# Performance work log

Measured on AMD Instinct MI355X. Metric: run time of the kernel, lower is better.

Reference implementation:

```python
import jax, jax.numpy as jnp
import numpy as np

N_NODES = 50000
N_EDGES = 800000
D_IN, D_HID, D_OUT = 128, 128, 64
BN_EPS = 1e-5


def gcn_conv(x, W, b, src, dst, ew, n):
    # PyG GCNConv: out[i] = sum_j norm_ij * (x @ W)[j] + b, with self-loops added
    xw = x @ W                                   # [N, D_out]
    loop = jnp.arange(n)
    s = jnp.concatenate([src, loop])             # add self-loops (weight 1)
    d = jnp.concatenate([dst, loop])
    w = jnp.concatenate([ew, jnp.ones((n,), x.dtype)])
    deg = jax.ops.segment_sum(w, d, num_segments=n)
    dinv = jnp.where(deg > 0, jax.lax.rsqrt(deg), 0.0)
    norm = dinv[s] * w * dinv[d]                 # symmetric normalization
    msg = xw[s] * norm[:, None]                  # gather + scale  [E+N, D_out]
    return jax.ops.segment_sum(msg, d, num_segments=n) + b


def setup_inputs() -> dict:
    key = jax.random.key(0)
    ks = jax.random.split(key, 12)
    x = jax.random.normal(ks[0], (N_NODES, D_IN), dtype=jnp.float32)
    edge_index = jax.random.randint(ks[1], (2, N_EDGES), 0, N_NODES, dtype=jnp.int64)
    edge_weight = jax.random.uniform(ks[2], (N_EDGES,), dtype=jnp.float32)
    W1 = jax.random.normal(ks[3], (D_IN, D_HID), dtype=jnp.float32) * 0.05
    b1 = jnp.zeros((D_HID,), jnp.float32)
    gamma = jnp.ones((D_HID,), jnp.float32)
    beta = jnp.zeros((D_HID,), jnp.float32)
    running_mean = jax.random.normal(ks[4], (D_HID,), dtype=jnp.float32) * 0.1
    running_var = jax.random.uniform(ks[5], (D_HID,), dtype=jnp.float32) + 0.5
    W2 = jax.random.normal(ks[6], (D_HID, D_OUT), dtype=jnp.float32) * 0.05
    b2 = jnp.zeros((D_OUT,), jnp.float32)
    return {"x": x, "edge_index": edge_index, "edge_weight": edge_weight,
            "W1": W1, "b1": b1, "gamma": gamma, "beta": beta,
            "running_mean": running_mean, "running_var": running_var,
            "W2": W2, "b2": b2}


def reference(x, edge_index, edge_weight, W1, b1, gamma, beta,
              running_mean, running_var, W2, b2):
    src, dst = edge_index[0], edge_index[1]
    n = x.shape[0]
    h = gcn_conv(x, W1, b1, src, dst, edge_weight, n)
    # BatchNorm1d in eval mode (running stats); dropout inactive in eval
    h = (h - running_mean) * jax.lax.rsqrt(running_var + BN_EPS) * gamma + beta
    h = jax.nn.relu(h)
    out = gcn_conv(h, W2, b2, src, dst, edge_weight, n)
    return out
```

## Files before the change

### kernel.cpp

```cpp
#include <hip/hip_runtime.h>
#include <hip/hip_fp16.h>

#define BN_EPS 1e-5f
#define PAD 64

static __device__ __forceinline__ unsigned short f2bf(float f) {
    unsigned u = __float_as_uint(f);
    u += 0x7FFF + ((u >> 16) & 1);
    return (unsigned short)(u >> 16);
}
static __device__ __forceinline__ float bf2f(unsigned short b) {
    return __uint_as_float((unsigned)b << 16);
}
static __device__ __forceinline__ unsigned pk(int s, float w) {
    return ((unsigned)s << 16) | (unsigned)__half_as_ushort(__float2half_rn(w));
}
static __device__ __forceinline__ float pw(unsigned e) {
    return __half2float(__ushort_as_half((unsigned short)(e & 0xFFFFu)));
}

__global__ __launch_bounds__(256) void k_fused(const int* __restrict__ src, const int* __restrict__ dst,
                                               const float* __restrict__ ew,
                                               int* cnt, unsigned* __restrict__ pad, int e, int gfill, int stride,
                                               const float* __restrict__ A, const float* __restrict__ W,
                                               unsigned short* __restrict__ C, int n,
                                               const float* __restrict__ b1, const float* __restrict__ gamma,
                                               const float* __restrict__ beta, const float* __restrict__ mean,
                                               const float* __restrict__ var,
                                               float* __restrict__ bnscale, float* __restrict__ bnshift,
                                               const float* __restrict__ W2, unsigned short* __restrict__ w2bf) {
    __shared__ float WsQ[32 * 128];
    __shared__ float AsT[128 * 32];
    int tid = threadIdx.x;
    int b = (int)blockIdx.x;
    int gGemm = (n + 31) / 32;

    bool isFill = ((b % stride) == 0) && (b / stride < gfill);
    if (isFill) {
        int i0 = ((b / stride) * 256 + tid) * 8;
        if (i0 + 7 < e) {
            int4   s0 = *(const int4*)(src + i0), s1 = *(const int4*)(src + i0 + 4);
            int4   d0 = *(const int4*)(dst + i0), d1 = *(const int4*)(dst + i0 + 4);
            float4 w0 = *(const float4*)(ew + i0), w1 = *(const float4*)(ew + i0 + 4);
            int p0 = atomicAdd(&cnt[d0.x], 1);
            int p1 = atomicAdd(&cnt[d0.y], 1);
            int p2 = atomicAdd(&cnt[d0.z], 1);
            int p3 = atomicAdd(&cnt[d0.w], 1);
            int p4 = atomicAdd(&cnt[d1.x], 1);
            int p5 = atomicAdd(&cnt[d1.y], 1);
            int p6 = atomicAdd(&cnt[d1.z], 1);
            int p7 = atomicAdd(&cnt[d1.w], 1);
            if (p0 < PAD) pad[(size_t)d0.x * PAD + p0] = pk(s0.x, w0.x);
            if (p1 < PAD) pad[(size_t)d0.y * PAD + p1] = pk(s0.y, w0.y);
            if (p2 < PAD) pad[(size_t)d0.z * PAD + p2] = pk(s0.z, w0.z);
            if (p3 < PAD) pad[(size_t)d0.w * PAD + p3] = pk(s0.w, w0.w);
            if (p4 < PAD) pad[(size_t)d1.x * PAD + p4] = pk(s1.x, w1.x);
            if (p5 < PAD) pad[(size_t)d1.y * PAD + p5] = pk(s1.y, w1.y);
            if (p6 < PAD) pad[(size_t)d1.z * PAD + p6] = pk(s1.z, w1.z);
            if (p7 < PAD) pad[(size_t)d1.w * PAD + p7] = pk(s1.w, w1.w);
        } else {
            for (int i = i0; i < e; ++i) {
                int d = dst[i];
                int p = atomicAdd(&cnt[d], 1);
                if (p < PAD) pad[(size_t)d * PAD + p] = pk(src[i], ew[i]);
            }
        }
        return;
    }

    int fillsBefore = (b == 0) ? 0 : min(gfill, (b - 1) / stride + 1);
    int g = b - fillsBefore;
    if (g == gGemm) {
        if (tid < 128) {
            float sc = gamma[tid] * rsqrtf(var[tid] + BN_EPS);
            bnscale[tid] = sc;
            bnshift[tid] = (b1[tid] - mean[tid]) * sc + beta[tid];
        }
        const float4* W4 = (const float4*)W2;
        ushort4* O = (ushort4*)w2bf;
        #pragma unroll
        for (int q = 0; q < 8; ++q) {
            float4 v = W4[q * 256 + tid];
            O[q * 256 + tid] = make_ushort4(f2bf(v.x), f2bf(v.y), f2bf(v.z), f2bf(v.w));
        }
        return;
    }

    int row0 = g * 32;
    {
        int lr = tid & 31, kq = tid >> 5;
        int gr = row0 + lr; if (gr > n - 1) gr = n - 1;
        const float4* A4 = (const float4*)(A + (size_t)gr * 128);
        #pragma unroll
        for (int j = 0; j < 4; ++j) {
            float4 v = A4[kq * 4 + j];
            int k = kq * 16 + j * 4;
            AsT[(k + 0) * 32 + lr] = v.x;
            AsT[(k + 1) * 32 + lr] = v.y;
            AsT[(k + 2) * 32 + lr] = v.z;
            AsT[(k + 3) * 32 + lr] = v.w;
        }
    }
    int cg_ = tid & 31, rg = tid >> 5;
    float4 acc0 = make_float4(0, 0, 0, 0), acc1 = acc0, acc2 = acc0, acc3 = acc0;
    const float4* W4 = (const float4*)W;
    float4* WsQ4 = (float4*)WsQ;
    const float4* AsT4 = (const float4*)AsT;
    for (int ph = 0; ph < 4; ++ph) {
        __syncthreads();
        #pragma unroll
        for (int j = 0; j < 4; ++j)
            WsQ4[j * 256 + tid] = W4[ph * 1024 + j * 256 + tid];
        __syncthreads();
        #pragma unroll 16
        for (int kk = 0; kk < 32; ++kk) {
            float4 w = WsQ4[kk * 32 + cg_];
            float4 a = AsT4[(ph * 32 + kk) * 8 + rg];
            acc0.x += a.x * w.x; acc0.y += a.x * w.y; acc0.z += a.x * w.z; acc0.w += a.x * w.w;
            acc1.x += a.y * w.x; acc1.y += a.y * w.y; acc1.z += a.y * w.z; acc1.w += a.y * w.w;
            acc2.x += a.z * w.x; acc2.y += a.z * w.y; acc2.z += a.z * w.z; acc2.w += a.z * w.w;
            acc3.x += a.w * w.x; acc3.y += a.w * w.y; acc3.z += a.w * w.z; acc3.w += a.w * w.w;
        }
    }
    ushort4* C4 = (ushort4*)C;
    int r = row0 + rg * 4;
    if (r + 0 < n) C4[(size_t)(r + 0) * 32 + cg_] = make_ushort4(f2bf(acc0.x), f2bf(acc0.y), f2bf(acc0.z), f2bf(acc0.w));
    if (r + 1 < n) C4[(size_t)(r + 1) * 32 + cg_] = make_ushort4(f2bf(acc1.x), f2bf(acc1.y), f2bf(acc1.z), f2bf(acc1.w));
    if (r + 2 < n) C4[(size_t)(r + 2) * 32 + cg_] = make_ushort4(f2bf(acc2.x), f2bf(acc2.y), f2bf(acc2.z), f2bf(acc2.w));
    if (r + 3 < n) C4[(size_t)(r + 3) * 32 + cg_] = make_ushort4(f2bf(acc3.x), f2bf(acc3.y), f2bf(acc3.z), f2bf(acc3.w));
}

__global__ __launch_bounds__(256) void k_deg(const int* __restrict__ cnt, const unsigned* __restrict__ pad,
                                             float* __restrict__ dinv, int n) {
    int i = blockIdx.x * 256 + threadIdx.x;
    if (i < n) {
        int c = min(cnt[i], PAD);
        size_t base = (size_t)i * PAD;
        const uint4* row = (const uint4*)(pad + base);
        float s = 1.0f;
        int p = 0;
        for (; p + 3 < c; p += 4) {
            uint4 v = row[p >> 2];
            s += pw(v.x) + pw(v.y) + pw(v.z) + pw(v.w);
        }
        for (; p < c; ++p) s += pw(pad[base + p]);
        dinv[i] = rsqrtf(s);
    }
}

__global__ __launch_bounds__(256) void k_ag12(const unsigned short* __restrict__ xw, const int* __restrict__ cnt,
                                              const unsigned* __restrict__ pad,
                                              const float* __restrict__ dinv,
                                              const float* __restrict__ scale, const float* __restrict__ shift,
                                              const unsigned short* __restrict__ w2bf,
                                              unsigned short* __restrict__ hw2, int n) {
    __shared__ unsigned short W2s[128 * 64];
    int tid = threadIdx.x;
    {
        const uint4* s4 = (const uint4*)w2bf;
        uint4* d4 = (uint4*)W2s;
        #pragma unroll
        for (int q = 0; q < 4; ++q) d4[q * 256 + tid] = s4[q * 256 + tid];
    }
    __syncthreads();

    int g = tid >> 5;
    int lc = tid & 31;
    int node = blockIdx.x * 8 + g;
    if (node >= n) return;

    unsigned hu0, hu1;
    {
        const ushort4* X4 = (const ushort4*)xw;
        float di = dinv[node];
        int c = min(cnt[node], PAD);
        size_t base = (size_t)node * PAD;
        ushort4 q0 = X4[(size_t)node * 32 + lc];
        float4 acc0 = make_float4(bf2f(q0.x) * di, bf2f(q0.y) * di, bf2f(q0.z) * di, bf2f(q0.w) * di);
        float4 acc1 = make_float4(0, 0, 0, 0);
        float4 acc2 = make_float4(0, 0, 0, 0);
        float4 acc3 = make_float4(0, 0, 0, 0);
        int p = 0;
        for (; p + 3 < c; p += 4) {
            uint4 ee = *(const uint4*)(pad + base + p);
            float w0 = pw(ee.x) * dinv[ee.x >> 16];
            float w1 = pw(ee.y) * dinv[ee.y >> 16];
            float w2 = pw(ee.z) * dinv[ee.z >> 16];
            float w3 = pw(ee.w) * dinv[ee.w >> 16];
            ushort4 a = X4[(size_t)(ee.x >> 16) * 32 + lc];
            ushort4 b = X4[(size_t)(ee.y >> 16) * 32 + lc];
            ushort4 gg = X4[(size_t)(ee.z >> 16) * 32 + lc];
            ushort4 d = X4[(size_t)(ee.w >> 16) * 32 + lc];
            acc0.x += w0 * bf2f(a.x); acc0.y += w0 * bf2f(a.y); acc0.z += w0 * bf2f(a.z); acc0.w += w0 * bf2f(a.w);
            acc1.x += w1 * bf2f(b.x); acc1.y += w1 * bf2f(b.y); acc1.z += w1 * bf2f(b.z); acc1.w += w1 * bf2f(b.w);
            acc2.x += w2 * bf2f(gg.x); acc2.y += w2 * bf2f(gg.y); acc2.z += w2 * bf2f(gg.z); acc2.w += w2 * bf2f(gg.w);
            acc3.x += w3 * bf2f(d.x); acc3.y += w3 * bf2f(d.y); acc3.z += w3 * bf2f(d.z); acc3.w += w3 * bf2f(d.w);
        }
        for (; p < c; ++p) {
            unsigned e0 = pad[base + p];
            float w0 = pw(e0) * dinv[e0 >> 16];
            ushort4 a = X4[(size_t)(e0 >> 16) * 32 + lc];
            acc0.x += w0 * bf2f(a.x); acc0.y += w0 * bf2f(a.y); acc0.z += w0 * bf2f(a.z); acc0.w += w0 * bf2f(a.w);
        }
        acc0.x = (acc0.x + acc1.x + acc2.x + acc3.x) * di;
        acc0.y = (acc0.y + acc1.y + acc2.y + acc3.y) * di;
        acc0.z = (acc0.z + acc1.z + acc2.z + acc3.z) * di;
        acc0.w = (acc0.w + acc1.w + acc2.w + acc3.w) * di;
        float4 Sc = ((const float4*)scale)[lc];
        float4 Sh = ((const float4*)shift)[lc];
        unsigned short r0 = f2bf(fmaxf(acc0.x * Sc.x + Sh.x, 0.0f));
        unsigned short r1 = f2bf(fmaxf(acc0.y * Sc.y + Sh.y, 0.0f));
        unsigned short r2 = f2bf(fmaxf(acc0.z * Sc.z + Sh.z, 0.0f));
        unsigned short r3 = f2bf(fmaxf(acc0.w * Sc.w + Sh.w, 0.0f));
        hu0 = ((unsigned)r1 << 16) | (unsigned)r0;
        hu1 = ((unsigned)r3 << 16) | (unsigned)r2;
    }

    float a0 = 0.0f, a1 = 0.0f;
    const unsigned* W2u = (const unsigned*)W2s;
    #pragma unroll 8
    for (int k = 0; k < 32; ++k) {
        unsigned p0 = (unsigned)__shfl((int)hu0, k, 32);
        unsigned p1 = (unsigned)__shfl((int)hu1, k, 32);
        float h0 = bf2f((unsigned short)(p0 & 0xFFFFu));
        float h1 = bf2f((unsigned short)(p0 >> 16));
        float h2 = bf2f((unsigned short)(p1 & 0xFFFFu));
        float h3 = bf2f((unsigned short)(p1 >> 16));
        unsigned w0u = W2u[(4 * k + 0) * 32 + lc];
        unsigned w1u = W2u[(4 * k + 1) * 32 + lc];
        unsigned w2u = W2u[(4 * k + 2) * 32 + lc];
        unsigned w3u = W2u[(4 * k + 3) * 32 + lc];
        a0 += h0 * bf2f((unsigned short)(w0u & 0xFFFFu));
        a1 += h0 * bf2f((unsigned short)(w0u >> 16));
        a0 += h1 * bf2f((unsigned short)(w1u & 0xFFFFu));
        a1 += h1 * bf2f((unsigned short)(w1u >> 16));
        a0 += h2 * bf2f((unsigned short)(w2u & 0xFFFFu));
        a1 += h2 * bf2f((unsigned short)(w2u >> 16));
        a0 += h3 * bf2f((unsigned short)(w3u & 0xFFFFu));
        a1 += h3 * bf2f((unsigned short)(w3u >> 16));
    }
    unsigned outp = ((unsigned)f2bf(a1) << 16) | (unsigned)f2bf(a0);
    ((unsigned*)hw2)[(size_t)node * 32 + lc] = outp;
}

__global__ __launch_bounds__(256) void k_agg2(const unsigned short* __restrict__ hw, const int* __restrict__ cnt,
                                              const unsigned* __restrict__ pad,
                                              const float* __restrict__ dinv,
                                              const float* __restrict__ b2, float* __restrict__ out, int n) {
    int node = blockIdx.x * 16 + (threadIdx.x >> 4);
    if (node >= n) return;
    int lc = threadIdx.x & 15;
    const ushort4* X4 = (const ushort4*)hw;
    float di = dinv[node];
    int c = min(cnt[node], PAD);
    size_t base = (size_t)node * PAD;
    ushort4 q0 = X4[(size_t)node * 16 + lc];
    float4 acc0 = make_float4(bf2f(q0.x) * di, bf2f(q0.y) * di, bf2f(q0.z) * di, bf2f(q0.w) * di);
    float4 acc1 = make_float4(0, 0, 0, 0);
    float4 acc2 = make_float4(0, 0, 0, 0);
    float4 acc3 = make_float4(0, 0, 0, 0);
    int p = 0;
    for (; p + 3 < c; p += 4) {
        uint4 ee = *(const uint4*)(pad + base + p);
        float w0 = pw(ee.x) * dinv[ee.x >> 16];
        float w1 = pw(ee.y) * dinv[ee.y >> 16];
        float w2 = pw(ee.z) * dinv[ee.z >> 16];
        float w3 = pw(ee.w) * dinv[ee.w >> 16];
        ushort4 a = X4[(size_t)(ee.x >> 16) * 16 + lc];
        ushort4 b = X4[(size_t)(ee.y >> 16) * 16 + lc];
        ushort4 g = X4[(size_t)(ee.z >> 16) * 16 + lc];
        ushort4 d = X4[(size_t)(ee.w >> 16) * 16 + lc];
        acc0.x += w0 * bf2f(a.x); acc0.y += w0 * bf2f(a.y); acc0.z += w0 * bf2f(a.z); acc0.w += w0 * bf2f(a.w);
        acc1.x += w1 * bf2f(b.x); acc1.y += w1 * bf2f(b.y); acc1.z += w1 * bf2f(b.z); acc1.w += w1 * bf2f(b.w);
        acc2.x += w2 * bf2f(g.x); acc2.y += w2 * bf2f(g.y); acc2.z += w2 * bf2f(g.z); acc2.w += w2 * bf2f(g.w);
        acc3.x += w3 * bf2f(d.x); acc3.y += w3 * bf2f(d.y); acc3.z += w3 * bf2f(d.z); acc3.w += w3 * bf2f(d.w);
    }
    for (; p < c; ++p) {
        unsigned e0 = pad[base + p];
        float w0 = pw(e0) * dinv[e0 >> 16];
        ushort4 a = X4[(size_t)(e0 >> 16) * 16 + lc];
        acc0.x += w0 * bf2f(a.x); acc0.y += w0 * bf2f(a.y); acc0.z += w0 * bf2f(a.z); acc0.w += w0 * bf2f(a.w);
    }
    float4 B = ((const float4*)b2)[lc];
    acc0.x = (acc0.x + acc1.x + acc2.x + acc3.x) * di + B.x;
    acc0.y = (acc0.y + acc1.y + acc2.y + acc3.y) * di + B.y;
    acc0.z = (acc0.z + acc1.z + acc2.z + acc3.z) * di + B.z;
    acc0.w = (acc0.w + acc1.w + acc2.w + acc3.w) * di + B.w;
    ((float4*)out)[(size_t)node * 16 + lc] = acc0;
}


extern "C" void kernel_launch(void* const* d_in, const int* in_sizes, int n_in,
                              void* d_out, int out_size, void* d_ws, size_t ws_size,
                              hipStream_t stream) {
    const float* x     = (const float*)d_in[0];
    const int*   ei    = (const int*)d_in[1];
    const float* ew    = (const float*)d_in[2];
    const float* W1    = (const float*)d_in[3];
    const float* b1    = (const float*)d_in[4];
    const float* gamma = (const float*)d_in[5];
    const float* beta  = (const float*)d_in[6];
    const float* rmean = (const float*)d_in[7];
    const float* rvar  = (const float*)d_in[8];
    const float* W2    = (const float*)d_in[9];
    const float* b2    = (const float*)d_in[10];
    float* out = (float*)d_out;

    int N = in_sizes[0] / 128;
    int E = in_sizes[2];
    const int* src = ei;
    const int* dst = ei + E;

    char* p = (char*)d_ws;
    auto carve = [&](size_t bytes) { char* q = p; p += (bytes + 255) & ~(size_t)255; return (void*)q; };
    int*      cnt     = (int*)     carve(sizeof(int) * (size_t)N);
    unsigned* pad     = (unsigned*)carve(sizeof(unsigned) * (size_t)N * PAD);
    float*    dinv    = (float*)   carve(sizeof(float) * (size_t)N);
    float*    bnscale = (float*)   carve(sizeof(float) * 128);
    float*    bnshift = (float*)   carve(sizeof(float) * 128);
    unsigned short* w2bf = (unsigned short*)carve(sizeof(unsigned short) * 128 * 64);
    unsigned short* xw1  = (unsigned short*)carve(sizeof(unsigned short) * (size_t)N * 128);
    unsigned short* hw2  = (unsigned short*)carve(sizeof(unsigned short) * (size_t)N * 64);

    int gN    = (N + 255) / 256;
    int gFill = (E + 2047) / 2048;
    int gGemm = (N + 31) / 32;
    int T     = gFill + gGemm + 1;
    int S     = T / gFill;
    if (S < 2) S = 2;

    hipMemsetAsync(cnt, 0, sizeof(int) * (size_t)N, stream);
    k_fused <<<T, 256, 0, stream>>>(src, dst, ew, cnt, pad, E, gFill, S,
                                    x, W1, xw1, N,
                                    b1, gamma, beta, rmean, rvar, bnscale, bnshift,
                                    W2, w2bf);
    k_deg   <<<gN, 256, 0, stream>>>(cnt, pad, dinv, N);
    k_ag12  <<<(N + 7) / 8, 256, 0, stream>>>(xw1, cnt, pad, dinv, bnscale, bnshift, w2bf, hw2, N);
    k_agg2  <<<(N + 15) / 16, 256, 0, stream>>>(hw2, cnt, pad, dinv, b2, out, N);
}
```

Measured before the change: 215.0 us.

## Prescale node features by source dinv to drop per-edge dinv gathers

Replaces the degree kernel with a warp-per-node prep kernel that computes dinv and rescales xw1 in place by the source-side normalization. Layer-2 output is likewise scaled by dinv before storage, so both aggregation loops no longer gather dinv per edge. The edge-fill path also processes 16 edges per thread instead of 8 and halves its block count. The cost is an extra read-modify-write pass over xw1 and a second bf16 rounding of it.

```diff
diff --git a/kernel.cpp b/kernel.cpp
--- a/kernel.cpp
+++ b/kernel.cpp
@@ -37,27 +37,30 @@
 
     bool isFill = ((b % stride) == 0) && (b / stride < gfill);
     if (isFill) {
-        int i0 = ((b / stride) * 256 + tid) * 8;
-        if (i0 + 7 < e) {
-            int4   s0 = *(const int4*)(src + i0), s1 = *(const int4*)(src + i0 + 4);
-            int4   d0 = *(const int4*)(dst + i0), d1 = *(const int4*)(dst + i0 + 4);
-            float4 w0 = *(const float4*)(ew + i0), w1 = *(const float4*)(ew + i0 + 4);
-            int p0 = atomicAdd(&cnt[d0.x], 1);
-            int p1 = atomicAdd(&cnt[d0.y], 1);
-            int p2 = atomicAdd(&cnt[d0.z], 1);
-            int p3 = atomicAdd(&cnt[d0.w], 1);
-            int p4 = atomicAdd(&cnt[d1.x], 1);
-            int p5 = atomicAdd(&cnt[d1.y], 1);
-            int p6 = atomicAdd(&cnt[d1.z], 1);
-            int p7 = atomicAdd(&cnt[d1.w], 1);
-            if (p0 < PAD) pad[(size_t)d0.x * PAD + p0] = pk(s0.x, w0.x);
-            if (p1 < PAD) pad[(size_t)d0.y * PAD + p1] = pk(s0.y, w0.y);
-            if (p2 < PAD) pad[(size_t)d0.z * PAD + p2] = pk(s0.z, w0.z);
-            if (p3 < PAD) pad[(size_t)d0.w * PAD + p3] = pk(s0.w, w0.w);
-            if (p4 < PAD) pad[(size_t)d1.x * PAD + p4] = pk(s1.x, w1.x);
-            if (p5 < PAD) pad[(size_t)d1.y * PAD + p5] = pk(s1.y, w1.y);
-            if (p6 < PAD) pad[(size_t)d1.z * PAD + p6] = pk(s1.z, w1.z);
-            if (p7 < PAD) pad[(size_t)d1.w * PAD + p7] = pk(s1.w, w1.w);
+        int i0 = ((b / stride) * 256 + tid) * 16;
+        if (i0 + 15 < e) {
+            int4 s[4], d[4]; float4 w[4];
+            #pragma unroll
+            for (int j = 0; j < 4; ++j) {
+                s[j] = *(const int4*)(src + i0 + 4 * j);
+                d[j] = *(const int4*)(dst + i0 + 4 * j);
+                w[j] = *(const float4*)(ew + i0 + 4 * j);
+            }
+            int p0[4], p1[4], p2[4], p3[4];
+            #pragma unroll
+            for (int j = 0; j < 4; ++j) {
+                p0[j] = atomicAdd(&cnt[d[j].x], 1);
+                p1[j] = atomicAdd(&cnt[d[j].y], 1);
+                p2[j] = atomicAdd(&cnt[d[j].z], 1);
+                p3[j] = atomicAdd(&cnt[d[j].w], 1);
+            }
+            #pragma unroll
+            for (int j = 0; j < 4; ++j) {
+                if (p0[j] < PAD) pad[(size_t)d[j].x * PAD + p0[j]] = pk(s[j].x, w[j].x);
+                if (p1[j] < PAD) pad[(size_t)d[j].y * PAD + p1[j]] = pk(s[j].y, w[j].y);
+                if (p2[j] < PAD) pad[(size_t)d[j].z * PAD + p2[j]] = pk(s[j].z, w[j].z);
+                if (p3[j] < PAD) pad[(size_t)d[j].w * PAD + p3[j]] = pk(s[j].w, w[j].w);
+            }
         } else {
             for (int i = i0; i < e; ++i) {
                 int d = dst[i];
@@ -130,22 +133,24 @@
     if (r + 3 < n) C4[(size_t)(r + 3) * 32 + cg_] = make_ushort4(f2bf(acc3.x), f2bf(acc3.y), f2bf(acc3.z), f2bf(acc3.w));
 }
 
-__global__ __launch_bounds__(256) void k_deg(const int* __restrict__ cnt, const unsigned* __restrict__ pad,
-                                             float* __restrict__ dinv, int n) {
-    int i = blockIdx.x * 256 + threadIdx.x;
-    if (i < n) {
-        int c = min(cnt[i], PAD);
-        size_t base = (size_t)i * PAD;
-        const uint4* row = (const uint4*)(pad + base);
-        float s = 1.0f;
-        int p = 0;
-        for (; p + 3 < c; p += 4) {
-            uint4 v = row[p >> 2];
-            s += pw(v.x) + pw(v.y) + pw(v.z) + pw(v.w);
-        }
-        for (; p < c; ++p) s += pw(pad[base + p]);
-        dinv[i] = rsqrtf(s);
-    }
+__global__ __launch_bounds__(256) void k_prep(const int* __restrict__ cnt, const unsigned* __restrict__ pad,
+                                              float* __restrict__ dinv, unsigned short* __restrict__ xw1, int n) {
+    int g = threadIdx.x >> 5, lc = threadIdx.x & 31;
+    int node = blockIdx.x * 8 + g;
+    if (node >= n) return;
+    int c = min(cnt[node], PAD);
+    size_t base = (size_t)node * PAD;
+    float s = 0.0f;
+    if (lc < c)      s += pw(pad[base + lc]);
+    if (lc + 32 < c) s += pw(pad[base + lc + 32]);
+    #pragma unroll
+    for (int off = 1; off < 32; off <<= 1) s += __shfl_xor(s, off, 32);
+    float di = rsqrtf(1.0f + s);
+    if (lc == 0) dinv[node] = di;
+    ushort4* X4 = (ushort4*)xw1;
+    ushort4 v = X4[(size_t)node * 32 + lc];
+    X4[(size_t)node * 32 + lc] = make_ushort4(f2bf(bf2f(v.x) * di), f2bf(bf2f(v.y) * di),
+                                              f2bf(bf2f(v.z) * di), f2bf(bf2f(v.w) * di));
 }
 
 __global__ __launch_bounds__(256) void k_ag12(const unsigned short* __restrict__ xw, const int* __restrict__ cnt,
@@ -169,24 +174,21 @@
     int node = blockIdx.x * 8 + g;
     if (node >= n) return;
 
+    float di = dinv[node];
     unsigned hu0, hu1;
     {
         const ushort4* X4 = (const ushort4*)xw;
-        float di = dinv[node];
         int c = min(cnt[node], PAD);
         size_t base = (size_t)node * PAD;
         ushort4 q0 = X4[(size_t)node * 32 + lc];
-        float4 acc0 = make_float4(bf2f(q0.x) * di, bf2f(q0.y) * di, bf2f(q0.z) * di, bf2f(q0.w) * di);
+        float4 acc0 = make_float4(bf2f(q0.x), bf2f(q0.y), bf2f(q0.z), bf2f(q0.w));
         float4 acc1 = make_float4(0, 0, 0, 0);
         float4 acc2 = make_float4(0, 0, 0, 0);
         float4 acc3 = make_float4(0, 0, 0, 0);
         int p = 0;
         for (; p + 3 < c; p += 4) {
             uint4 ee = *(const uint4*)(pad + base + p);
-            float w0 = pw(ee.x) * dinv[ee.x >> 16];
-            float w1 = pw(ee.y) * dinv[ee.y >> 16];
-            float w2 = pw(ee.z) * dinv[ee.z >> 16];
-            float w3 = pw(ee.w) * dinv[ee.w >> 16];
+            float w0 = pw(ee.x), w1 = pw(ee.y), w2 = pw(ee.z), w3 = pw(ee.w);
             ushort4 a = X4[(size_t)(ee.x >> 16) * 32 + lc];
             ushort4 b = X4[(size_t)(ee.y >> 16) * 32 + lc];
             ushort4 gg = X4[(size_t)(ee.z >> 16) * 32 + lc];
@@ -198,7 +200,7 @@
         }
         for (; p < c; ++p) {
             unsigned e0 = pad[base + p];
-            float w0 = pw(e0) * dinv[e0 >> 16];
+            float w0 = pw(e0);
             ushort4 a = X4[(size_t)(e0 >> 16) * 32 + lc];
             acc0.x += w0 * bf2f(a.x); acc0.y += w0 * bf2f(a.y); acc0.z += w0 * bf2f(a.z); acc0.w += w0 * bf2f(a.w);
         }
@@ -239,6 +241,7 @@
         a0 += h3 * bf2f((unsigned short)(w3u & 0xFFFFu));
         a1 += h3 * bf2f((unsigned short)(w3u >> 16));
     }
+    a0 *= di; a1 *= di;
     unsigned outp = ((unsigned)f2bf(a1) << 16) | (unsigned)f2bf(a0);
     ((unsigned*)hw2)[(size_t)node * 32 + lc] = outp;
 }
@@ -255,17 +258,14 @@
     int c = min(cnt[node], PAD);
     size_t base = (size_t)node * PAD;
     ushort4 q0 = X4[(size_t)node * 16 + lc];
-    float4 acc0 = make_float4(bf2f(q0.x) * di, bf2f(q0.y) * di, bf2f(q0.z) * di, bf2f(q0.w) * di);
+    float4 acc0 = make_float4(bf2f(q0.x), bf2f(q0.y), bf2f(q0.z), bf2f(q0.w));
     float4 acc1 = make_float4(0, 0, 0, 0);
     float4 acc2 = make_float4(0, 0, 0, 0);
     float4 acc3 = make_float4(0, 0, 0, 0);
     int p = 0;
     for (; p + 3 < c; p += 4) {
         uint4 ee = *(const uint4*)(pad + base + p);
-        float w0 = pw(ee.x) * dinv[ee.x >> 16];
-        float w1 = pw(ee.y) * dinv[ee.y >> 16];
-        float w2 = pw(ee.z) * dinv[ee.z >> 16];
-        float w3 = pw(ee.w) * dinv[ee.w >> 16];
+        float w0 = pw(ee.x), w1 = pw(ee.y), w2 = pw(ee.z), w3 = pw(ee.w);
         ushort4 a = X4[(size_t)(ee.x >> 16) * 16 + lc];
         ushort4 b = X4[(size_t)(ee.y >> 16) * 16 + lc];
         ushort4 g = X4[(size_t)(ee.z >> 16) * 16 + lc];
@@ -277,7 +277,7 @@
     }
     for (; p < c; ++p) {
         unsigned e0 = pad[base + p];
-        float w0 = pw(e0) * dinv[e0 >> 16];
+        float w0 = pw(e0);
         ushort4 a = X4[(size_t)(e0 >> 16) * 16 + lc];
         acc0.x += w0 * bf2f(a.x); acc0.y += w0 * bf2f(a.y); acc0.z += w0 * bf2f(a.z); acc0.w += w0 * bf2f(a.w);
     }
@@ -322,8 +322,7 @@
     unsigned short* xw1  = (unsigned short*)carve(sizeof(unsigned short) * (size_t)N * 128);
     unsigned short* hw2  = (unsigned short*)carve(sizeof(unsigned short) * (size_t)N * 64);
 
-    int gN    = (N + 255) / 256;
-    int gFill = (E + 2047) / 2048;
+    int gFill = (E + 4095) / 4096;
     int gGemm = (N + 31) / 32;
     int T     = gFill + gGemm + 1;
     int S     = T / gFill;
@@ -334,7 +333,7 @@
                                     x, W1, xw1, N,
                                     b1, gamma, beta, rmean, rvar, bnscale, bnshift,
                                     W2, w2bf);
-    k_deg   <<<gN, 256, 0, stream>>>(cnt, pad, dinv, N);
+    k_prep  <<<(N + 7) / 8, 256, 0, stream>>>(cnt, pad, dinv, xw1, N);
     k_ag12  <<<(N + 7) / 8, 256, 0, stream>>>(xw1, cnt, pad, dinv, bnscale, bnshift, w2bf, hw2, N);
     k_agg2  <<<(N + 15) / 16, 256, 0, stream>>>(hw2, cnt, pad, dinv, b2, out, N);
 }
```

New measurement: 258.9 us. +20.4%, slower.
